# Kernel tuning notes

Hardware: AMD Instinct MI355X
Metric: run time of the kernel (lower is better)

Reference implementation:

```python
import jax, jax.numpy as jnp
import numpy as np

E = 8           # num experts
TOPK = 2
NUM_TOKENS = 4096
K = 2048        # hidden dim
N = 2816        # intermediate dim
P = NUM_TOKENS * TOPK   # num_valid_tokens (token, expert-slot) pairs
PE = P // E             # pairs per expert (token-sorted, equal load)


def setup_inputs() -> dict:
    key = jax.random.key(0)
    ks = jax.random.split(key, 6)
    x = jax.random.normal(ks[0], (NUM_TOKENS, K), dtype=jnp.float32)
    W1 = jax.random.normal(ks[1], (E, N, K), dtype=jnp.float32) * (K ** -0.5)  # gate proj
    W3 = jax.random.normal(ks[2], (E, N, K), dtype=jnp.float32) * (K ** -0.5)  # up proj
    W2 = jax.random.normal(ks[3], (E, K, N), dtype=jnp.float32) * (N ** -0.5)  # down proj
    topk_weights = jax.random.uniform(ks[4], (P,), dtype=jnp.float32)          # router weights per pair
    sorted_token_ids = jax.random.randint(ks[5], (P,), 0, NUM_TOKENS, dtype=jnp.int32)
    # token-sorted dispatch: pairs grouped by expert, equal count per expert
    expert_ids = jnp.repeat(jnp.arange(E, dtype=jnp.int32), PE)
    return {"x": x, "W1": W1, "W3": W3, "W2": W2,
            "topk_weights": topk_weights,
            "sorted_token_ids": sorted_token_ids,
            "expert_ids": expert_ids}


def reference(x, W1, W3, W2, topk_weights, sorted_token_ids, expert_ids):
    # Pairs are grouped by expert (token-sorted dispatch), PE pairs per expert.
    eids = expert_ids.reshape(E, PE)[:, 0]            # expert id per group
    xg = x[sorted_token_ids].reshape(E, PE, K)        # gather token activations per pair
    gate = jnp.einsum('epk,enk->epn', xg, W1[eids])   # [E, PE, N]
    up = jnp.einsum('epk,enk->epn', xg, W3[eids])     # [E, PE, N]
    # kernel computes sigmoid(gate) * up (as written in the triton body)
    h = jax.nn.sigmoid(gate) * up
    out_p = jnp.einsum('epn,ekn->epk', h, W2[eids])   # down proj, [E, PE, K]
    out_p = out_p * topk_weights.reshape(E, PE, 1)
    # scatter-add per-pair results into per-token output (atomic_add in kernel)
    out = jnp.zeros((x.shape[0], K), dtype=x.dtype)
    out = out.at[sorted_token_ids].add(out_p.reshape(P, K))
    return out
```

## Files before the change

### kernel.cpp

```cpp
#include <hip/hip_runtime.h>
#include <hip/hip_bf16.h>
#include <cstdint>

typedef __bf16 bf16_t;
typedef __attribute__((ext_vector_type(8))) __bf16 bf16x8;
typedef __attribute__((ext_vector_type(4))) __bf16 bf16x4;
typedef __attribute__((ext_vector_type(4))) float f32x4;

#define NEXP 8
#define DK   2048
#define DN   2816
#define DN2  5632
#define NP   8192
#define PPE  1024

__global__ void k_cvt(const float* __restrict__ src, bf16_t* __restrict__ dst, int total4) {
    int stride = gridDim.x * blockDim.x;
    for (int i = blockIdx.x * blockDim.x + threadIdx.x; i < total4; i += stride) {
        float4 v = reinterpret_cast<const float4*>(src)[i];
        bf16x4 o = { (bf16_t)v.x, (bf16_t)v.y, (bf16_t)v.z, (bf16_t)v.w };
        reinterpret_cast<bf16x4*>(dst)[i] = o;
    }
}

__global__ void k_cvt_w13(const float* __restrict__ src, bf16_t* __restrict__ dst, int rowAdd) {
    int stride = gridDim.x * blockDim.x;
    const int total4 = NEXP * DN * (DK / 4);
    for (int i = blockIdx.x * blockDim.x + threadIdx.x; i < total4; i += stride) {
        int g  = i >> 9;
        int c4 = i & 511;
        int e  = g / DN;
        int n  = g - e * DN;
        long drow = (long)e * DN2 + ((n >> 4) << 5) + (n & 15) + rowAdd;
        float4 v = reinterpret_cast<const float4*>(src)[i];
        bf16x4 o = { (bf16_t)v.x, (bf16_t)v.y, (bf16_t)v.z, (bf16_t)v.w };
        *reinterpret_cast<bf16x4*>(dst + drow * DK + c4 * 4) = o;
    }
}

__global__ void k_gather(const float* __restrict__ x, const int* __restrict__ ids,
                         bf16_t* __restrict__ xg) {
    int i = blockIdx.x * blockDim.x + threadIdx.x;
    if (i >= NP * (DK / 4)) return;
    int p  = i >> 9;
    int c4 = i & 511;
    int tok = ids[p];
    float4 v = reinterpret_cast<const float4*>(x + (size_t)tok * DK)[c4];
    bf16x4 o = { (bf16_t)v.x, (bf16_t)v.y, (bf16_t)v.z, (bf16_t)v.w };
    *reinterpret_cast<bf16x4*>(xg + (size_t)p * DK + c4 * 4) = o;
}

__device__ __forceinline__ void gl2lds16(const bf16_t* g, bf16_t* l) {
    __builtin_amdgcn_global_load_lds(
        (__attribute__((address_space(1))) void*)(const_cast<bf16_t*>(g)),
        (__attribute__((address_space(3))) void*)(l), 16, 0, 0);
}

#define BARX() __builtin_amdgcn_s_barrier()
#define LGKM0() asm volatile("s_waitcnt lgkmcnt(0)" ::: "memory")
#define VMW4() asm volatile("s_waitcnt vmcnt(4)" ::: "memory")
#define VMW0() asm volatile("s_waitcnt vmcnt(0)" ::: "memory")

#define STG(ARR, SRC, LD, BUF, HALF, KT) do {                                   \
    gl2lds16((SRC) + (long)((HALF) * 128) * (LD) + (long)(KT) * 64,             \
             &ARR[BUF][(HALF) * 128 + w8][0]);                                  \
    gl2lds16((SRC) + (long)((HALF) * 128 + 64) * (LD) + (long)(KT) * 64,        \
             &ARR[BUF][(HALF) * 128 + 64 + w8][0]);                             \
} while (0)

#define LOADA(DST, BASE) do { _Pragma("unroll")                                 \
    for (int mi_ = 0; mi_ < 4; ++mi_) {                                         \
        DST[mi_][0] = *reinterpret_cast<const bf16x8*>((BASE) + aoff0 + mi_ * 1024); \
        DST[mi_][1] = *reinterpret_cast<const bf16x8*>((BASE) + aoff1 + mi_ * 1024); \
    } } while (0)

#define LOADB(DST, BASE) do { _Pragma("unroll")                                 \
    for (int ni_ = 0; ni_ < 2; ++ni_) {                                         \
        DST[ni_][0] = *reinterpret_cast<const bf16x8*>((BASE) + boff0 + ni_ * 1024); \
        DST[ni_][1] = *reinterpret_cast<const bf16x8*>((BASE) + boff1 + ni_ * 1024); \
    } } while (0)

#define MFMAQ(AF, BF, MIB, NIB) do {                                            \
    __builtin_amdgcn_s_setprio(1);                                              \
    _Pragma("unroll") for (int kk_ = 0; kk_ < 2; ++kk_)                         \
    _Pragma("unroll") for (int mi_ = 0; mi_ < 4; ++mi_)                         \
    _Pragma("unroll") for (int ni_ = 0; ni_ < 2; ++ni_)                         \
        acc[(MIB) + mi_][(NIB) + ni_] = __builtin_amdgcn_mfma_f32_16x16x32_bf16( \
            AF[mi_][kk_], BF[ni_][kk_], acc[(MIB) + mi_][(NIB) + ni_], 0, 0, 0); \
    __builtin_amdgcn_s_setprio(0);                                              \
} while (0)

template <int EPI>
__launch_bounds__(512, 2)
__global__ void k_gemm(const bf16_t* __restrict__ A, const bf16_t* __restrict__ B,
                       bf16_t* __restrict__ Hout, float* __restrict__ Fout,
                       const float* __restrict__ tw, const int* __restrict__ ids,
                       int Mtiles, int Ntiles, int nkt, int lda, int ldb,
                       long aStride, long bStride) {
    __shared__ bf16_t As[2][256][64];
    __shared__ bf16_t Bs[2][256][64];

    const int nwg = gridDim.x;
    const int logical = (blockIdx.x & 7) * (nwg >> 3) + (blockIdx.x >> 3);
    const int tpe = Mtiles * Ntiles;
    const int e  = logical / tpe;
    const int r  = logical - e * tpe;
    const int mt = r / Ntiles;
    const int nt = r - mt * Ntiles;

    const int tid  = threadIdx.x;
    const int w    = tid >> 6;
    const int w8   = w * 8;
    const int lane = tid & 63;
    const int wr = w >> 2, wc = w & 3;
    const int fr = lane & 15;
    const int fc = lane >> 4;

    const int srow = tid >> 3;
    const int schk = (tid & 7) ^ (srow & 7);
    const bf16_t* aSrc = A + (long)e * aStride + ((long)mt * 256 + srow) * lda + schk * 8;
    const bf16_t* bSrc = B + (long)e * bStride + ((long)nt * 256 + srow) * ldb + schk * 8;

    const int sx = lane & 7;
    const int aoff0 = (wr * 128 + fr) * 64 + ((0 + fc) ^ sx) * 8;
    const int aoff1 = (wr * 128 + fr) * 64 + ((4 + fc) ^ sx) * 8;
    const int boff0 = (wc * 64 + fr) * 64 + ((0 + fc) ^ sx) * 8;
    const int boff1 = (wc * 64 + fr) * 64 + ((4 + fc) ^ sx) * 8;

    const bf16_t* As0 = &As[0][0][0];
    const bf16_t* As1 = &As[1][0][0];
    const bf16_t* Bs0 = &Bs[0][0][0];
    const bf16_t* Bs1 = &Bs[1][0][0];

    f32x4 acc[8][4];
#pragma unroll
    for (int a = 0; a < 8; ++a)
#pragma unroll
        for (int b = 0; b < 4; ++b) acc[a][b] = (f32x4){0.f, 0.f, 0.f, 0.f};

    bf16x8 af[4][2], ah[4][2], bl[2][2], bh[2][2];

    STG(As, aSrc, lda, 0, 0, 0); STG(As, aSrc, lda, 0, 1, 0);
    STG(Bs, bSrc, ldb, 0, 0, 0); STG(Bs, bSrc, ldb, 0, 1, 0);
    STG(Bs, bSrc, ldb, 1, 0, 1); STG(Bs, bSrc, ldb, 1, 1, 1);
    VMW4();
    BARX();

    const int nIter = nkt >> 1;
    for (int it = 0; it < nIter; ++it) {
        const int t = it * 2;
        const bool last = (it == nIter - 1);
        LOADA(af, As0); LOADB(bl, Bs0);
        STG(As, aSrc, lda, 1, 0, t + 1);
        BARX(); LGKM0();
        MFMAQ(af, bl, 0, 0);
        BARX();
        LOADB(bh, Bs0 + 2048);
        STG(As, aSrc, lda, 1, 1, t + 1);
        BARX(); LGKM0();
        MFMAQ(af, bh, 0, 2);
        BARX();
        LOADA(ah, As0 + 4096);
        if (!last) STG(Bs, bSrc, ldb, 0, 0, t + 2);
        BARX(); LGKM0();
        MFMAQ(ah, bh, 4, 2);
        BARX();
        if (!last) { STG(Bs, bSrc, ldb, 0, 1, t + 2); VMW4(); } else { VMW0(); }
        BARX();
        MFMAQ(ah, bl, 4, 0);
        BARX();
        LOADA(af, As1); LOADB(bl, Bs1);
        if (!last) STG(As, aSrc, lda, 0, 0, t + 2);
        BARX(); LGKM0();
        MFMAQ(af, bl, 0, 0);
        BARX();
        LOADB(bh, Bs1 + 2048);
        if (!last) STG(As, aSrc, lda, 0, 1, t + 2);
        BARX(); LGKM0();
        MFMAQ(af, bh, 0, 2);
        BARX();
        LOADA(ah, As1 + 4096);
        if (!last) STG(Bs, bSrc, ldb, 1, 0, t + 3);
        BARX(); LGKM0();
        MFMAQ(ah, bh, 4, 2);
        BARX();
        if (!last) { STG(Bs, bSrc, ldb, 1, 1, t + 3); VMW4(); } else { VMW0(); }
        BARX();
        MFMAQ(ah, bl, 4, 0);
        BARX();
    }

    if constexpr (EPI == 0) {
        const long prow0 = (long)e * PPE + (long)mt * 256 + wr * 128 + fc * 4;
        const int col0 = nt * 128 + wc * 32 + fr;
#pragma unroll
        for (int mi = 0; mi < 8; ++mi)
#pragma unroll
            for (int i = 0; i < 4; ++i) {
                long row = prow0 + mi * 16 + i;
#pragma unroll
                for (int p = 0; p < 2; ++p) {
                    float g = acc[mi][2 * p][i];
                    float u = acc[mi][2 * p + 1][i];
                    float s = 1.f / (1.f + __expf(-g));
                    Hout[row * DN + col0 + p * 16] = (bf16_t)(s * u);
                }
            }
    } else {
        const int p0 = e * PPE + mt * 256 + wr * 128 + fc * 4;
        const int col0 = nt * 256 + wc * 64 + fr;
#pragma unroll
        for (int mi = 0; mi < 8; ++mi)
#pragma unroll
            for (int i = 0; i < 4; ++i) {
                int gp = p0 + mi * 16 + i;
                float wgt = tw[gp];
                float* ob = Fout + (long)ids[gp] * DK + col0;
#pragma unroll
                for (int ni = 0; ni < 4; ++ni)
                    atomicAdd(ob + ni * 16, acc[mi][ni][i] * wgt);
            }
    }
}

extern "C" void kernel_launch(void* const* d_in, const int* in_sizes, int n_in,
                              void* d_out, int out_size, void* d_ws, size_t ws_size,
                              hipStream_t stream) {
    const float* x   = (const float*)d_in[0];
    const float* W1  = (const float*)d_in[1];
    const float* W3  = (const float*)d_in[2];
    const float* W2  = (const float*)d_in[3];
    const float* tw  = (const float*)d_in[4];
    const int*   sid = (const int*)d_in[5];
    float* out = (float*)d_out;

    char* ws = (char*)d_ws;
    bf16_t* w13i = (bf16_t*)ws;
    bf16_t* w2b  = (bf16_t*)(ws + 184549376L);
    bf16_t* xg   = (bf16_t*)(ws + 276824064L);
    bf16_t* h    = (bf16_t*)(ws + 310378496L);

    hipMemsetAsync(d_out, 0, (size_t)out_size * sizeof(float), stream);

    k_cvt_w13<<<2048, 256, 0, stream>>>(W1, w13i, 0);
    k_cvt_w13<<<2048, 256, 0, stream>>>(W3, w13i, 16);
    k_cvt<<<2048, 256, 0, stream>>>(W2, w2b, NEXP * DK * (DN / 4));
    k_gather<<<NP * (DK / 4) / 256, 256, 0, stream>>>(x, sid, xg);

    k_gemm<0><<<NEXP * 4 * 22, 512, 0, stream>>>(
        xg, w13i, h, nullptr, nullptr, nullptr,
        4, 22, 32, DK, DK, (long)PPE * DK, (long)DN2 * DK);

    k_gemm<1><<<NEXP * 4 * 8, 512, 0, stream>>>(
        h, w2b, nullptr, out, tw, sid,
        4, 8, 44, DN, DN, (long)PPE * DN, (long)DK * DN);
}
```

Measured before the change: 507.8 us.

## Overlap W2 conversion with first GEMM and restage GEMM prefetch order

The W2 fp32-to-bf16 conversion now runs inside extra workgroups appended to the gate/up GEMM launch, so it overlaps with GEMM work instead of running as a separate kernel. The W1 and W3 conversions are merged into a single launch. In the GEMM main loop, global-to-LDS stages are reordered so both B halves issue together and A halves shift one slot earlier, with vmcnt raised to 6 and an lgkmcnt(8) wait added. The extra conversion blocks share the GPU with GEMM tiles and can contend for bandwidth, and the new wait counts must match the real number of outstanding loads.

```diff
diff --git a/kernel.cpp b/kernel.cpp
--- a/kernel.cpp
+++ b/kernel.cpp
@@ -14,25 +14,19 @@
 #define NP   8192
 #define PPE  1024
 
-__global__ void k_cvt(const float* __restrict__ src, bf16_t* __restrict__ dst, int total4) {
+__global__ void k_cvt_w13(const float* __restrict__ W1, const float* __restrict__ W3,
+                          bf16_t* __restrict__ dst) {
+    const int total4 = NEXP * DN * (DK / 4);
     int stride = gridDim.x * blockDim.x;
-    for (int i = blockIdx.x * blockDim.x + threadIdx.x; i < total4; i += stride) {
-        float4 v = reinterpret_cast<const float4*>(src)[i];
-        bf16x4 o = { (bf16_t)v.x, (bf16_t)v.y, (bf16_t)v.z, (bf16_t)v.w };
-        reinterpret_cast<bf16x4*>(dst)[i] = o;
-    }
-}
-
-__global__ void k_cvt_w13(const float* __restrict__ src, bf16_t* __restrict__ dst, int rowAdd) {
-    int stride = gridDim.x * blockDim.x;
-    const int total4 = NEXP * DN * (DK / 4);
-    for (int i = blockIdx.x * blockDim.x + threadIdx.x; i < total4; i += stride) {
-        int g  = i >> 9;
-        int c4 = i & 511;
-        int e  = g / DN;
-        int n  = g - e * DN;
-        long drow = (long)e * DN2 + ((n >> 4) << 5) + (n & 15) + rowAdd;
-        float4 v = reinterpret_cast<const float4*>(src)[i];
+    for (int i = blockIdx.x * blockDim.x + threadIdx.x; i < 2 * total4; i += stride) {
+        int sel = i >= total4;
+        int j   = sel ? i - total4 : i;
+        int g   = j >> 9;
+        int c4  = j & 511;
+        int e   = g / DN;
+        int n   = g - e * DN;
+        long drow = (long)e * DN2 + ((n >> 4) << 5) + (n & 15) + (sel ? 16 : 0);
+        float4 v = reinterpret_cast<const float4*>(sel ? W3 : W1)[j];
         bf16x4 o = { (bf16_t)v.x, (bf16_t)v.y, (bf16_t)v.z, (bf16_t)v.w };
         *reinterpret_cast<bf16x4*>(dst + drow * DK + c4 * 4) = o;
     }
@@ -56,10 +50,11 @@
         (__attribute__((address_space(3))) void*)(l), 16, 0, 0);
 }
 
-#define BARX() __builtin_amdgcn_s_barrier()
+#define BARX()  __builtin_amdgcn_s_barrier()
 #define LGKM0() asm volatile("s_waitcnt lgkmcnt(0)" ::: "memory")
-#define VMW4() asm volatile("s_waitcnt vmcnt(4)" ::: "memory")
-#define VMW0() asm volatile("s_waitcnt vmcnt(0)" ::: "memory")
+#define LGKM8() asm volatile("s_waitcnt lgkmcnt(8)" ::: "memory")
+#define VMW6()  asm volatile("s_waitcnt vmcnt(6)" ::: "memory")
+#define VMW0()  asm volatile("s_waitcnt vmcnt(0)" ::: "memory")
 
 #define STG(ARR, SRC, LD, BUF, HALF, KT) do {                                   \
     gl2lds16((SRC) + (long)((HALF) * 128) * (LD) + (long)(KT) * 64,             \
@@ -96,12 +91,26 @@
                        bf16_t* __restrict__ Hout, float* __restrict__ Fout,
                        const float* __restrict__ tw, const int* __restrict__ ids,
                        int Mtiles, int Ntiles, int nkt, int lda, int ldb,
-                       long aStride, long bStride) {
+                       long aStride, long bStride, int nGemm,
+                       const float* __restrict__ cvtSrc, bf16_t* __restrict__ cvtDst,
+                       int cvtN4) {
     __shared__ bf16_t As[2][256][64];
     __shared__ bf16_t Bs[2][256][64];
 
     const int nwg = gridDim.x;
     const int logical = (blockIdx.x & 7) * (nwg >> 3) + (blockIdx.x >> 3);
+
+    if (logical >= nGemm) {
+        int base = (logical - nGemm) * (int)blockDim.x + (int)threadIdx.x;
+        int stride = (nwg - nGemm) * (int)blockDim.x;
+        for (int i = base; i < cvtN4; i += stride) {
+            float4 v = reinterpret_cast<const float4*>(cvtSrc)[i];
+            bf16x4 o = { (bf16_t)v.x, (bf16_t)v.y, (bf16_t)v.z, (bf16_t)v.w };
+            reinterpret_cast<bf16x4*>(cvtDst)[i] = o;
+        }
+        return;
+    }
+
     const int tpe = Mtiles * Ntiles;
     const int e  = logical / tpe;
     const int r  = logical - e * tpe;
@@ -140,10 +149,11 @@
 
     bf16x8 af[4][2], ah[4][2], bl[2][2], bh[2][2];
 
+    STG(Bs, bSrc, ldb, 0, 0, 0); STG(Bs, bSrc, ldb, 0, 1, 0);
     STG(As, aSrc, lda, 0, 0, 0); STG(As, aSrc, lda, 0, 1, 0);
-    STG(Bs, bSrc, ldb, 0, 0, 0); STG(Bs, bSrc, ldb, 0, 1, 0);
     STG(Bs, bSrc, ldb, 1, 0, 1); STG(Bs, bSrc, ldb, 1, 1, 1);
-    VMW4();
+    STG(As, aSrc, lda, 1, 0, 1);
+    VMW6();
     BARX();
 
     const int nIter = nkt >> 1;
@@ -151,40 +161,40 @@
         const int t = it * 2;
         const bool last = (it == nIter - 1);
         LOADA(af, As0); LOADB(bl, Bs0);
-        STG(As, aSrc, lda, 1, 0, t + 1);
+        STG(As, aSrc, lda, 1, 1, t + 1);
+        LGKM8();
         BARX(); LGKM0();
         MFMAQ(af, bl, 0, 0);
         BARX();
         LOADB(bh, Bs0 + 2048);
-        STG(As, aSrc, lda, 1, 1, t + 1);
         BARX(); LGKM0();
         MFMAQ(af, bh, 0, 2);
         BARX();
         LOADA(ah, As0 + 4096);
-        if (!last) STG(Bs, bSrc, ldb, 0, 0, t + 2);
+        if (!last) { STG(Bs, bSrc, ldb, 0, 0, t + 2); STG(Bs, bSrc, ldb, 0, 1, t + 2); }
         BARX(); LGKM0();
         MFMAQ(ah, bh, 4, 2);
         BARX();
-        if (!last) { STG(Bs, bSrc, ldb, 0, 1, t + 2); VMW4(); } else { VMW0(); }
+        if (!last) { STG(As, aSrc, lda, 0, 0, t + 2); VMW6(); } else { VMW0(); }
         BARX();
         MFMAQ(ah, bl, 4, 0);
         BARX();
         LOADA(af, As1); LOADB(bl, Bs1);
-        if (!last) STG(As, aSrc, lda, 0, 0, t + 2);
+        if (!last) STG(As, aSrc, lda, 0, 1, t + 2);
+        LGKM8();
         BARX(); LGKM0();
         MFMAQ(af, bl, 0, 0);
         BARX();
         LOADB(bh, Bs1 + 2048);
-        if (!last) STG(As, aSrc, lda, 0, 1, t + 2);
         BARX(); LGKM0();
         MFMAQ(af, bh, 0, 2);
         BARX();
         LOADA(ah, As1 + 4096);
-        if (!last) STG(Bs, bSrc, ldb, 1, 0, t + 3);
+        if (!last) { STG(Bs, bSrc, ldb, 1, 0, t + 3); STG(Bs, bSrc, ldb, 1, 1, t + 3); }
         BARX(); LGKM0();
         MFMAQ(ah, bh, 4, 2);
         BARX();
-        if (!last) { STG(Bs, bSrc, ldb, 1, 1, t + 3); VMW4(); } else { VMW0(); }
+        if (!last) { STG(As, aSrc, lda, 1, 0, t + 3); VMW6(); } else { VMW0(); }
         BARX();
         MFMAQ(ah, bl, 4, 0);
         BARX();
@@ -242,16 +252,16 @@
 
     hipMemsetAsync(d_out, 0, (size_t)out_size * sizeof(float), stream);
 
-    k_cvt_w13<<<2048, 256, 0, stream>>>(W1, w13i, 0);
-    k_cvt_w13<<<2048, 256, 0, stream>>>(W3, w13i, 16);
-    k_cvt<<<2048, 256, 0, stream>>>(W2, w2b, NEXP * DK * (DN / 4));
+    k_cvt_w13<<<2048, 256, 0, stream>>>(W1, W3, w13i);
     k_gather<<<NP * (DK / 4) / 256, 256, 0, stream>>>(x, sid, xg);
 
-    k_gemm<0><<<NEXP * 4 * 22, 512, 0, stream>>>(
+    k_gemm<0><<<NEXP * 4 * 22 + 256, 512, 0, stream>>>(
         xg, w13i, h, nullptr, nullptr, nullptr,
-        4, 22, 32, DK, DK, (long)PPE * DK, (long)DN2 * DK);
+        4, 22, 32, DK, DK, (long)PPE * DK, (long)DN2 * DK,
+        NEXP * 4 * 22, W2, w2b, NEXP * DK * (DN / 4));
 
     k_gemm<1><<<NEXP * 4 * 8, 512, 0, stream>>>(
         h, w2b, nullptr, out, tw, sid,
-        4, 8, 44, DN, DN, (long)PPE * DN, (long)DK * DN);
-}
+        4, 8, 44, DN, DN, (long)PPE * DN, (long)DK * DN,
+        NEXP * 4 * 8, nullptr, nullptr, 0);
+}
```

Result: slower. 559.4 us (+10.2%).
